# Kernel optimization log

Measured on AMD Instinct MI355X. Metric: run time of the kernel, lower is better.

The kernel has to match this reference:

```python
import jax, jax.numpy as jnp
import numpy as np

N_NODES = 100000
N_REL = 8
IN_DIM = 64
HID = 128
OUT = 64
N_EDGES = 640000


def setup_inputs() -> dict:
    key = jax.random.key(0)
    ks = jax.random.split(key, 24)

    def w(k, shape, fan_in):
        return jax.random.normal(k, shape, jnp.float32) / np.sqrt(fan_in).astype(np.float32)

    inp = {}
    inp["emb"] = jax.random.normal(ks[0], (N_NODES, IN_DIM), jnp.float32)
    dims = [(IN_DIM, HID), (HID, HID), (HID, HID // 2), (HID // 2, OUT)]
    for i, (di, do) in enumerate(dims, 1):
        inp[f"W{i}"] = w(ks[3 * i], (N_REL, di, do), di)      # per-relation weight
        inp[f"R{i}"] = w(ks[3 * i + 1], (di, do), di)          # root weight
        inp[f"B{i}"] = jnp.zeros((do,), jnp.float32)           # bias
    inp["g1"] = jnp.ones((HID,), jnp.float32)
    inp["b1"] = jnp.zeros((HID,), jnp.float32)
    inp["g2"] = jnp.ones((HID,), jnp.float32)
    inp["b2"] = jnp.zeros((HID,), jnp.float32)
    inp["ei"] = jax.random.randint(ks[20], (2, N_EDGES), 0, N_NODES, jnp.int32)
    inp["et"] = jax.random.randint(ks[21], (N_EDGES,), 0, N_REL, jnp.int32)
    return inp


def rgcn(x, ei, et, W, Wr, b):
    # PyG RGCNConv (aggr='mean'): out_i = x_i @ Wroot + b + sum_r mean_{j in N_r(i)} x_j @ W_r
    # Aggregate-then-transform: mean x[src] per (dst, rel) bin, then per-relation GEMM.
    n, r, d = x.shape[0], W.shape[0], x.shape[1]
    src, dst = ei[0], ei[1]
    seg = dst * r + et                                   # combined (node, relation) segment id
    agg = jax.ops.segment_sum(x[src], seg, num_segments=n * r)          # [N*R, d]
    cnt = jax.ops.segment_sum(jnp.ones((src.shape[0],), x.dtype), seg, num_segments=n * r)
    agg = (agg / jnp.maximum(cnt, 1.0)[:, None]).reshape(n, r, d)       # mean per relation
    return jnp.einsum('nri,rio->no', agg, W) + x @ Wr + b


def layer_norm(x, g, b, eps=1e-5):
    mu = jnp.mean(x, axis=-1, keepdims=True)
    var = jnp.mean((x - mu) ** 2, axis=-1, keepdims=True)
    return (x - mu) * jax.lax.rsqrt(var + eps) * g + b


def reference(emb, W1, R1, B1, W2, R2, B2, W3, R3, B3, W4, R4, B4, g1, b1, g2, b2, ei, et):
    # dropout is eval-mode identity
    x = jax.nn.relu(rgcn(emb, ei, et, W1, R1, B1))
    x = layer_norm(x, g1, b1)
    identity = x
    x = jax.nn.relu(rgcn(x, ei, et, W2, R2, B2))
    x = layer_norm(x + identity, g2, b2)
    x = jax.nn.relu(rgcn(x, ei, et, W3, R3, B3))
    return rgcn(x, ei, et, W4, R4, B4)
```

## Files before the change

### kernel.cpp

```cpp
#include <hip/hip_runtime.h>
#include <math.h>

#define NN 100000
#define NR 8
#define NE 640000
#define SEGN (NN * NR)
#define SPB 2048
#define NSB ((SEGN + SPB - 1) / SPB)

#define TILES 1563
#define HT1 782
#define HT2 781
#define HP1 (HT1 * 64)
#define HP2 (HT2 * 64)
#define HPF (TILES * 64)

typedef __attribute__((ext_vector_type(8))) __bf16 bf16x8;
typedef __attribute__((ext_vector_type(4))) float  f32x4;

__device__ __forceinline__ float bf2f(unsigned short b) {
    return __uint_as_float((unsigned)b << 16);
}
__device__ __forceinline__ unsigned short f2bf(float v) {
    __bf16 b = (__bf16)v;
    return __builtin_bit_cast(unsigned short, b);
}


__global__ __launch_bounds__(256) void count_kernel(
    const int* __restrict__ dst, const int* __restrict__ et, unsigned* __restrict__ cnt) {
    int e = blockIdx.x * 256 + threadIdx.x;
    if (e < NE) atomicAdd(&cnt[(size_t)et[e] * NN + dst[e]], 1u);
}

__global__ __launch_bounds__(256) void scan1_kernel(
    const unsigned* __restrict__ cnt, unsigned* __restrict__ bsum) {
    __shared__ unsigned red[256];
    int b = blockIdx.x, t = threadIdx.x;
    int i0 = b * SPB;
    unsigned s = 0;
#pragma unroll
    for (int k = 0; k < SPB / 256; ++k) {
        int i = i0 + k * 256 + t;
        if (i < SEGN) s += cnt[i];
    }
    red[t] = s;
    __syncthreads();
    for (int off = 128; off >= 1; off >>= 1) {
        if (t < off) red[t] += red[t + off];
        __syncthreads();
    }
    if (t == 0) bsum[b] = red[0];
}

__global__ __launch_bounds__(512) void scan2_kernel(
    unsigned* __restrict__ bsum, int* __restrict__ segoff) {
    __shared__ unsigned buf[512];
    int t = threadIdx.x;
    unsigned v = (t < NSB) ? bsum[t] : 0u;
    buf[t] = v;
    __syncthreads();
    for (int off = 1; off < 512; off <<= 1) {
        unsigned w = (t >= off) ? buf[t - off] : 0u;
        __syncthreads();
        buf[t] += w;
        __syncthreads();
    }
    if (t < NSB) bsum[t] = buf[t] - v;
    if (t == 0) segoff[SEGN] = NE;
}

__global__ __launch_bounds__(256) void scan3_kernel(
    const unsigned* __restrict__ cnt, const unsigned* __restrict__ bsum,
    int* __restrict__ segoff) {
    __shared__ unsigned lc[SPB];
    __shared__ unsigned tsum[256];
    int b = blockIdx.x, t = threadIdx.x;
    int i0 = b * SPB;
#pragma unroll
    for (int k = 0; k < SPB / 256; ++k) {
        int i = i0 + k * 256 + t;
        lc[k * 256 + t] = (i < SEGN) ? cnt[i] : 0u;
    }
    __syncthreads();
    unsigned s = 0;
#pragma unroll
    for (int k = 0; k < 8; ++k) s += lc[t * 8 + k];
    tsum[t] = s;
    __syncthreads();
    for (int off = 1; off < 256; off <<= 1) {
        unsigned w = (t >= off) ? tsum[t - off] : 0u;
        __syncthreads();
        tsum[t] += w;
        __syncthreads();
    }
    unsigned base = bsum[b] + tsum[t] - s;
#pragma unroll
    for (int k = 0; k < 8; ++k) {
        unsigned c = lc[t * 8 + k];
        lc[t * 8 + k] = base;
        base += c;
    }
    __syncthreads();
#pragma unroll
    for (int k = 0; k < SPB / 256; ++k) {
        int i = i0 + k * 256 + t;
        if (i < SEGN) segoff[i] = (int)lc[k * 256 + t];
    }
}

__global__ __launch_bounds__(256) void fill_kernel(
    const int* __restrict__ src, const int* __restrict__ dst, const int* __restrict__ et,
    const int* __restrict__ segoff, unsigned* __restrict__ cursor, int* __restrict__ esrc) {
    int e = blockIdx.x * 256 + threadIdx.x;
    if (e >= NE) return;
    int seg = et[e] * NN + dst[e];
    int pos = segoff[seg] + (int)atomicAdd(&cursor[seg], 1u);
    esrc[pos] = src[e];
}


template <int D, int O>
__global__ __launch_bounds__(256) void pack_kernel(
    const float* __restrict__ W, const float* __restrict__ Wr, __bf16* __restrict__ Wp) {
    constexpr int KT = D / 32, NTN = O / 16;
    int idx = blockIdx.x * 256 + threadIdx.x;
    if (idx >= (NR + 1) * KT * NTN * 64) return;
    int l = idx & 63;
    int rest = idx >> 6;
    int nt = rest % NTN; rest /= NTN;
    int kt = rest % KT;
    int r  = rest / KT;
    const float* srcw = (r < NR) ? (W + (size_t)r * D * O) : Wr;
    int n  = nt * 16 + (l & 15);
    int k0 = kt * 32 + (l >> 4) * 8;
    bf16x8 v;
#pragma unroll
    for (int j = 0; j < 8; ++j) v[j] = (__bf16)srcw[(size_t)(k0 + j) * O + n];
    *(bf16x8*)(Wp + (size_t)idx * 8) = v;
}


template <int D, int XF>
__global__ __launch_bounds__(256) void gather_kernel(
    const void* __restrict__ xin, const int* __restrict__ segoff,
    const int* __restrict__ esrc, ushort* __restrict__ agg,
    int base, int HP)
{
    int wv = threadIdx.x >> 6, ln = threadIdx.x & 63;
    int r  = blockIdx.y;
    int i0 = blockIdx.x * 16 + wv * 4;
    int n0 = base + i0;

    const float*   xf = (const float*)xin;
    const ushort*  xb = (const ushort*)xin;
    const ushort2* xs = (const ushort2*)xin;

    if (r < 8) {
        float ax[4] = {0, 0, 0, 0}, ay[4] = {0, 0, 0, 0};
        int eo[5];
#pragma unroll
        for (int k = 0; k <= 4; ++k) {
            int node = n0 + k; if (node > NN) node = NN;
            eo[k] = segoff[r * NN + node];
        }
        for (int ei = eo[0]; ei < eo[4]; ei += 4) {
            int nb = eo[4] - ei; if (nb > 4) nb = 4;
            int ss[4]; float vx[4], vy[4];
#pragma unroll
            for (int b = 0; b < 4; ++b) ss[b] = (b < nb) ? esrc[ei + b] : 0;
#pragma unroll
            for (int b = 0; b < 4; ++b) {
                if (b < nb) {
                    if constexpr (XF == 0) {
                        vx[b] = xf[(size_t)ss[b] * 64 + ln];
                    } else if constexpr (XF == 1) {
                        ushort2 w = xs[(size_t)ss[b] * 64 + ln];
                        vx[b] = bf2f(w.x); vy[b] = bf2f(w.y);
                    } else {
                        vx[b] = bf2f(xb[(size_t)ss[b] * 64 + ln]);
                    }
                }
            }
#pragma unroll
            for (int b = 0; b < 4; ++b) {
                if (b < nb) {
                    int e = ei + b;
                    int k = (e >= eo[1]) + (e >= eo[2]) + (e >= eo[3]);
#pragma unroll
                    for (int kk = 0; kk < 4; ++kk) {
                        ax[kk] += (kk == k) ? vx[b] : 0.0f;
                        if constexpr (D == 128) ay[kk] += (kk == k) ? vy[b] : 0.0f;
                    }
                }
            }
        }
#pragma unroll
        for (int k = 0; k < 4; ++k) {
            int c = eo[k + 1] - eo[k];
            float sc = (c > 0) ? 1.0f / (float)c : 0.0f;
            size_t row = ((size_t)r * HP + i0 + k) * D;
            agg[row + ln] = f2bf(ax[k] * sc);
            if constexpr (D == 128) agg[row + 64 + ln] = f2bf(ay[k] * sc);
        }
    } else {
#pragma unroll
        for (int k = 0; k < 4; ++k) {
            int n = n0 + k;
            float v0 = 0.0f, v1 = 0.0f;
            if (n < NN) {
                if constexpr (XF == 0) {
                    v0 = xf[(size_t)n * 64 + ln];
                } else if constexpr (XF == 1) {
                    ushort2 w = xs[(size_t)n * 64 + ln];
                    v0 = bf2f(w.x); v1 = bf2f(w.y);
                } else {
                    v0 = bf2f(xb[(size_t)n * 64 + ln]);
                }
            }
            size_t row = ((size_t)8 * HP + i0 + k) * D;
            agg[row + ln] = f2bf(v0);
            if constexpr (D == 128) agg[row + 64 + ln] = f2bf(v1);
        }
    }
}


template <int D, int O, int MODE, int OF>
__global__ __launch_bounds__(256) void gemm_layer(
    const ushort* __restrict__ agg, const __bf16* __restrict__ Wp,
    const float* __restrict__ bias, const float* __restrict__ gamma,
    const float* __restrict__ beta, void* __restrict__ outv,
    int base, int HP)
{
    constexpr int KT = D / 32, NTN = O / 16;
    int t = threadIdx.x, wv = t >> 6, ln = t & 63, lg = ln >> 4, lm = ln & 15;
    int i0 = blockIdx.x * 64;

    f32x4 acc[NTN];
#pragma unroll
    for (int nt = 0; nt < NTN; ++nt)
#pragma unroll
        for (int q = 0; q < 4; ++q) acc[nt][q] = 0.0f;

    const ushort* abase = agg + ((size_t)(i0 + wv * 16 + lm)) * D + lg * 8;

#pragma unroll 1
    for (int r = 0; r < 9; ++r) {
        const ushort* ar = abase + (size_t)r * HP * D;
        const __bf16* bp = Wp + (((size_t)(r * KT) * NTN) << 9) + (ln << 3);
#pragma unroll
        for (int kt = 0; kt < KT; ++kt) {
            bf16x8 A = *(const bf16x8*)(ar + kt * 32);
            const __bf16* bpk = bp + (((size_t)(kt * NTN)) << 9);
#pragma unroll
            for (int nt = 0; nt < NTN; ++nt) {
                bf16x8 B = *(const bf16x8*)(bpk + ((size_t)nt << 9));
                acc[nt] = __builtin_amdgcn_mfma_f32_16x16x32_bf16(A, B, acc[nt], 0, 0, 0);
            }
        }
    }

    float bb[NTN], gg[NTN], be[NTN];
#pragma unroll
    for (int nt = 0; nt < NTN; ++nt) {
        bb[nt] = bias[nt * 16 + lm];
        if constexpr (MODE <= 1) {
            gg[nt] = gamma[nt * 16 + lm];
            be[nt] = beta[nt * 16 + lm];
        } else {
            gg[nt] = 0.0f; be[nt] = 0.0f;
        }
    }
    const ushort* rootbase = agg + ((size_t)8 * HP + i0) * D;
#pragma unroll
    for (int q = 0; q < 4; ++q) {
        int row = wv * 16 + lg * 4 + q;
        int n = base + i0 + row;
        float v[NTN];
#pragma unroll
        for (int nt = 0; nt < NTN; ++nt) {
            v[nt] = acc[nt][q] + bb[nt];
            if constexpr (MODE <= 2) v[nt] = fmaxf(v[nt], 0.0f);
            if constexpr (MODE == 1)
                v[nt] += bf2f(rootbase[(size_t)row * D + nt * 16 + lm]);
        }
        if constexpr (MODE <= 1) {
            float s1 = 0.0f, s2 = 0.0f;
#pragma unroll
            for (int nt = 0; nt < NTN; ++nt) { s1 += v[nt]; s2 += v[nt] * v[nt]; }
#pragma unroll
            for (int off = 1; off < 16; off <<= 1) {
                s1 += __shfl_xor(s1, off, 64);
                s2 += __shfl_xor(s2, off, 64);
            }
            float mu  = s1 * (1.0f / O);
            float var = s2 * (1.0f / O) - mu * mu;
            float rs  = rsqrtf(var + 1e-5f);
#pragma unroll
            for (int nt = 0; nt < NTN; ++nt) v[nt] = (v[nt] - mu) * rs * gg[nt] + be[nt];
        }
        if (n < NN) {
            if constexpr (OF == 0) {
#pragma unroll
                for (int nt = 0; nt < NTN; ++nt)
                    ((float*)outv)[(size_t)n * O + nt * 16 + lm] = v[nt];
            } else if constexpr (OF == 1) {
#pragma unroll
                for (int nt = 0; nt < 4; ++nt)
                    ((ushort2*)outv)[(size_t)n * 64 + nt * 16 + lm] =
                        make_ushort2(f2bf(v[nt]), f2bf(v[nt + 4]));
            } else {
#pragma unroll
                for (int nt = 0; nt < NTN; ++nt)
                    ((ushort*)outv)[(size_t)n * 64 + nt * 16 + lm] = f2bf(v[nt]);
            }
        }
    }
}


extern "C" void kernel_launch(void* const* d_in, const int* in_sizes, int n_in,
                              void* d_out, int out_size, void* d_ws, size_t ws_size,
                              hipStream_t stream) {
    const float* emb = (const float*)d_in[0];
    const float* W1  = (const float*)d_in[1];
    const float* R1  = (const float*)d_in[2];
    const float* B1  = (const float*)d_in[3];
    const float* W2  = (const float*)d_in[4];
    const float* R2  = (const float*)d_in[5];
    const float* B2  = (const float*)d_in[6];
    const float* W3  = (const float*)d_in[7];
    const float* R3  = (const float*)d_in[8];
    const float* B3  = (const float*)d_in[9];
    const float* W4  = (const float*)d_in[10];
    const float* R4  = (const float*)d_in[11];
    const float* B4  = (const float*)d_in[12];
    const float* g1  = (const float*)d_in[13];
    const float* b1  = (const float*)d_in[14];
    const float* g2  = (const float*)d_in[15];
    const float* b2  = (const float*)d_in[16];
    const int*   ei  = (const int*)d_in[17];
    const int*   et  = (const int*)d_in[18];
    const int* srcp = ei;
    const int* dstp = ei + NE;

    char* ws = (char*)d_ws;
    if (ws_size < 185734160u) return;
    int*      segoff = (int*)(ws + 0);
    int*      esrc   = (int*)(ws + 3200016);
    __bf16*   Wp1    = (__bf16*)(ws + 5760016);
    __bf16*   Wp2    = (__bf16*)(ws + 5907472);
    __bf16*   Wp3    = (__bf16*)(ws + 6202384);
    __bf16*   Wp4    = (__bf16*)(ws + 6349840);
    void*     x1     = (void*)(ws + 6423568);
    void*     x2     = (void*)(ws + 32023568);
    void*     x3     = (void*)(ws + 57623568);
    ushort*   agg    = (ushort*)(ws + 70423568);
    unsigned* cnt    = (unsigned*)(ws + 70423568);
    unsigned* cursor = (unsigned*)(ws + 73623568);
    unsigned* bsum   = (unsigned*)(ws + 76823568);
    float*    outp   = (float*)d_out;

    hipMemsetAsync(cnt, 0, 3200000, stream);
    hipMemsetAsync(cursor, 0, 3200000, stream);

    count_kernel<<<(NE + 255) / 256, 256, 0, stream>>>(dstp, et, cnt);
    scan1_kernel<<<NSB, 256, 0, stream>>>(cnt, bsum);
    scan2_kernel<<<1, 512, 0, stream>>>(bsum, segoff);
    scan3_kernel<<<NSB, 256, 0, stream>>>(cnt, bsum, segoff);
    fill_kernel<<<(NE + 255) / 256, 256, 0, stream>>>(
        srcp, dstp, et, segoff, cursor, esrc);

    pack_kernel<64, 128><<<(9 * 2 * 8 * 64 + 255) / 256, 256, 0, stream>>>(W1, R1, Wp1);
    pack_kernel<128, 128><<<(9 * 4 * 8 * 64 + 255) / 256, 256, 0, stream>>>(W2, R2, Wp2);
    pack_kernel<128, 64><<<(9 * 4 * 4 * 64 + 255) / 256, 256, 0, stream>>>(W3, R3, Wp3);
    pack_kernel<64, 64><<<(9 * 2 * 4 * 64 + 255) / 256, 256, 0, stream>>>(W4, R4, Wp4);

    gather_kernel<64, 0><<<dim3(HPF / 16, 9), 256, 0, stream>>>(emb, segoff, esrc, agg, 0, HPF);
    gemm_layer<64, 128, 0, 1><<<TILES, 256, 0, stream>>>(agg, Wp1, B1, g1, b1, x1, 0, HPF);

    gather_kernel<128, 1><<<dim3(HP1 / 16, 9), 256, 0, stream>>>(x1, segoff, esrc, agg, 0, HP1);
    gemm_layer<128, 128, 1, 1><<<HT1, 256, 0, stream>>>(agg, Wp2, B2, g2, b2, x2, 0, HP1);
    gather_kernel<128, 1><<<dim3(HP2 / 16, 9), 256, 0, stream>>>(x1, segoff, esrc, agg, HP1, HP2);
    gemm_layer<128, 128, 1, 1><<<HT2, 256, 0, stream>>>(agg, Wp2, B2, g2, b2, x2, HP1, HP2);

    gather_kernel<128, 1><<<dim3(HP1 / 16, 9), 256, 0, stream>>>(x2, segoff, esrc, agg, 0, HP1);
    gemm_layer<128, 64, 2, 2><<<HT1, 256, 0, stream>>>(agg, Wp3, B3, nullptr, nullptr, x3, 0, HP1);
    gather_kernel<128, 1><<<dim3(HP2 / 16, 9), 256, 0, stream>>>(x2, segoff, esrc, agg, HP1, HP2);
    gemm_layer<128, 64, 2, 2><<<HT2, 256, 0, stream>>>(agg, Wp3, B3, nullptr, nullptr, x3, HP1, HP2);

    gather_kernel<64, 2><<<dim3(HPF / 16, 9), 256, 0, stream>>>(x3, segoff, esrc, agg, 0, HPF);
    gemm_layer<64, 64, 3, 0><<<TILES, 256, 0, stream>>>(agg, Wp4, B4, nullptr, nullptr, outp, 0, HPF);
}
```

Before: 824.7 us.

## Interleave bf16 feature layout, pack row index into edge source, use nontemporal memory ops

```diff
diff --git a/kernel.cpp b/kernel.cpp
--- a/kernel.cpp
+++ b/kernel.cpp
@@ -114,9 +114,10 @@
     const int* __restrict__ segoff, unsigned* __restrict__ cursor, int* __restrict__ esrc) {
     int e = blockIdx.x * 256 + threadIdx.x;
     if (e >= NE) return;
-    int seg = et[e] * NN + dst[e];
+    int d = dst[e];
+    int seg = et[e] * NN + d;
     int pos = segoff[seg] + (int)atomicAdd(&cursor[seg], 1u);
-    esrc[pos] = src[e];
+    esrc[pos] = src[e] | ((d & 3) << 17);
 }
 
 
@@ -136,7 +137,11 @@
     int k0 = kt * 32 + (l >> 4) * 8;
     bf16x8 v;
 #pragma unroll
-    for (int j = 0; j < 8; ++j) v[j] = (__bf16)srcw[(size_t)(k0 + j) * O + n];
+    for (int j = 0; j < 8; ++j) {
+        int p  = k0 + j;
+        int kd = (D == 128) ? ((p >> 1) + ((p & 1) << 6)) : p;
+        v[j] = (__bf16)srcw[(size_t)kd * O + n];
+    }
     *(bf16x8*)(Wp + (size_t)idx * 8) = v;
 }
 
@@ -152,9 +157,9 @@
     int i0 = blockIdx.x * 16 + wv * 4;
     int n0 = base + i0;
 
-    const float*   xf = (const float*)xin;
-    const ushort*  xb = (const ushort*)xin;
-    const ushort2* xs = (const ushort2*)xin;
+    const float*    xf = (const float*)xin;
+    const ushort*   xb = (const ushort*)xin;
+    const unsigned* xs = (const unsigned*)xin;
 
     if (r < 8) {
         float ax[4] = {0, 0, 0, 0}, ay[4] = {0, 0, 0, 0};
@@ -166,27 +171,28 @@
         }
         for (int ei = eo[0]; ei < eo[4]; ei += 4) {
             int nb = eo[4] - ei; if (nb > 4) nb = 4;
-            int ss[4]; float vx[4], vy[4];
-#pragma unroll
-            for (int b = 0; b < 4; ++b) ss[b] = (b < nb) ? esrc[ei + b] : 0;
+            int mm[4]; float vx[4], vy[4];
+#pragma unroll
+            for (int b = 0; b < 4; ++b) mm[b] = (b < nb) ? esrc[ei + b] : 0;
 #pragma unroll
             for (int b = 0; b < 4; ++b) {
                 if (b < nb) {
+                    int s = mm[b] & 0x1FFFF;
                     if constexpr (XF == 0) {
-                        vx[b] = xf[(size_t)ss[b] * 64 + ln];
+                        vx[b] = xf[(size_t)s * 64 + ln];
                     } else if constexpr (XF == 1) {
-                        ushort2 w = xs[(size_t)ss[b] * 64 + ln];
-                        vx[b] = bf2f(w.x); vy[b] = bf2f(w.y);
+                        unsigned w = xs[(size_t)s * 64 + ln];
+                        vx[b] = bf2f((unsigned short)(w & 0xFFFFu));
+                        vy[b] = bf2f((unsigned short)(w >> 16));
                     } else {
-                        vx[b] = bf2f(xb[(size_t)ss[b] * 64 + ln]);
+                        vx[b] = bf2f(xb[(size_t)s * 64 + ln]);
                     }
                 }
             }
 #pragma unroll
             for (int b = 0; b < 4; ++b) {
                 if (b < nb) {
-                    int e = ei + b;
-                    int k = (e >= eo[1]) + (e >= eo[2]) + (e >= eo[3]);
+                    int k = mm[b] >> 17;
 #pragma unroll
                     for (int kk = 0; kk < 4; ++kk) {
                         ax[kk] += (kk == k) ? vx[b] : 0.0f;
@@ -200,27 +206,30 @@
             int c = eo[k + 1] - eo[k];
             float sc = (c > 0) ? 1.0f / (float)c : 0.0f;
             size_t row = ((size_t)r * HP + i0 + k) * D;
-            agg[row + ln] = f2bf(ax[k] * sc);
-            if constexpr (D == 128) agg[row + 64 + ln] = f2bf(ay[k] * sc);
+            if constexpr (D == 128) {
+                unsigned st = (unsigned)f2bf(ax[k] * sc) | ((unsigned)f2bf(ay[k] * sc) << 16);
+                __builtin_nontemporal_store(st, (unsigned*)(agg + row) + ln);
+            } else {
+                __builtin_nontemporal_store(f2bf(ax[k] * sc), agg + row + ln);
+            }
         }
     } else {
 #pragma unroll
         for (int k = 0; k < 4; ++k) {
             int n = n0 + k;
-            float v0 = 0.0f, v1 = 0.0f;
-            if (n < NN) {
-                if constexpr (XF == 0) {
-                    v0 = xf[(size_t)n * 64 + ln];
-                } else if constexpr (XF == 1) {
-                    ushort2 w = xs[(size_t)n * 64 + ln];
-                    v0 = bf2f(w.x); v1 = bf2f(w.y);
-                } else {
-                    v0 = bf2f(xb[(size_t)n * 64 + ln]);
+            size_t row = ((size_t)8 * HP + i0 + k) * D;
+            if constexpr (D == 128) {
+                unsigned w = 0;
+                if (n < NN) w = xs[(size_t)n * 64 + ln];
+                __builtin_nontemporal_store(w, (unsigned*)(agg + row) + ln);
+            } else {
+                ushort w = 0;
+                if (n < NN) {
+                    if constexpr (XF == 0) w = f2bf(xf[(size_t)n * 64 + ln]);
+                    else                   w = xb[(size_t)n * 64 + ln];
                 }
-            }
-            size_t row = ((size_t)8 * HP + i0 + k) * D;
-            agg[row + ln] = f2bf(v0);
-            if constexpr (D == 128) agg[row + 64 + ln] = f2bf(v1);
+                __builtin_nontemporal_store(w, agg + row + ln);
+            }
         }
     }
 }
@@ -230,8 +239,8 @@
 __global__ __launch_bounds__(256) void gemm_layer(
     const ushort* __restrict__ agg, const __bf16* __restrict__ Wp,
     const float* __restrict__ bias, const float* __restrict__ gamma,
-    const float* __restrict__ beta, void* __restrict__ outv,
-    int base, int HP)
+    const float* __restrict__ beta, const unsigned* __restrict__ xres,
+    void* __restrict__ outv, int base, int HP)
 {
     constexpr int KT = D / 32, NTN = O / 16;
     int t = threadIdx.x, wv = t >> 6, ln = t & 63, lg = ln >> 4, lm = ln & 15;
@@ -251,7 +260,7 @@
         const __bf16* bp = Wp + (((size_t)(r * KT) * NTN) << 9) + (ln << 3);
 #pragma unroll
         for (int kt = 0; kt < KT; ++kt) {
-            bf16x8 A = *(const bf16x8*)(ar + kt * 32);
+            bf16x8 A = __builtin_nontemporal_load((const bf16x8*)(ar + kt * 32));
             const __bf16* bpk = bp + (((size_t)(kt * NTN)) << 9);
 #pragma unroll
             for (int nt = 0; nt < NTN; ++nt) {
@@ -272,18 +281,20 @@
             gg[nt] = 0.0f; be[nt] = 0.0f;
         }
     }
-    const ushort* rootbase = agg + ((size_t)8 * HP + i0) * D;
 #pragma unroll
     for (int q = 0; q < 4; ++q) {
         int row = wv * 16 + lg * 4 + q;
         int n = base + i0 + row;
+        int nc = (n < NN) ? n : 0;
         float v[NTN];
 #pragma unroll
         for (int nt = 0; nt < NTN; ++nt) {
             v[nt] = acc[nt][q] + bb[nt];
             if constexpr (MODE <= 2) v[nt] = fmaxf(v[nt], 0.0f);
-            if constexpr (MODE == 1)
-                v[nt] += bf2f(rootbase[(size_t)row * D + nt * 16 + lm]);
+            if constexpr (MODE == 1) {
+                unsigned w = xres[(size_t)nc * 64 + (nt & 3) * 16 + lm];
+                v[nt] += bf2f((unsigned short)((nt < 4) ? (w & 0xFFFFu) : (w >> 16)));
+            }
         }
         if constexpr (MODE <= 1) {
             float s1 = 0.0f, s2 = 0.0f;
@@ -304,12 +315,13 @@
             if constexpr (OF == 0) {
 #pragma unroll
                 for (int nt = 0; nt < NTN; ++nt)
-                    ((float*)outv)[(size_t)n * O + nt * 16 + lm] = v[nt];
+                    __builtin_nontemporal_store(
+                        v[nt], (float*)outv + (size_t)n * O + nt * 16 + lm);
             } else if constexpr (OF == 1) {
 #pragma unroll
                 for (int nt = 0; nt < 4; ++nt)
-                    ((ushort2*)outv)[(size_t)n * 64 + nt * 16 + lm] =
-                        make_ushort2(f2bf(v[nt]), f2bf(v[nt + 4]));
+                    ((unsigned*)outv)[(size_t)n * 64 + nt * 16 + lm] =
+                        (unsigned)f2bf(v[nt]) | ((unsigned)f2bf(v[nt + 4]) << 16);
             } else {
 #pragma unroll
                 for (int nt = 0; nt < NTN; ++nt)
@@ -378,18 +390,24 @@
     pack_kernel<64, 64><<<(9 * 2 * 4 * 64 + 255) / 256, 256, 0, stream>>>(W4, R4, Wp4);
 
     gather_kernel<64, 0><<<dim3(HPF / 16, 9), 256, 0, stream>>>(emb, segoff, esrc, agg, 0, HPF);
-    gemm_layer<64, 128, 0, 1><<<TILES, 256, 0, stream>>>(agg, Wp1, B1, g1, b1, x1, 0, HPF);
+    gemm_layer<64, 128, 0, 1><<<TILES, 256, 0, stream>>>(
+        agg, Wp1, B1, g1, b1, nullptr, x1, 0, HPF);
 
     gather_kernel<128, 1><<<dim3(HP1 / 16, 9), 256, 0, stream>>>(x1, segoff, esrc, agg, 0, HP1);
-    gemm_layer<128, 128, 1, 1><<<HT1, 256, 0, stream>>>(agg, Wp2, B2, g2, b2, x2, 0, HP1);
+    gemm_layer<128, 128, 1, 1><<<HT1, 256, 0, stream>>>(
+        agg, Wp2, B2, g2, b2, (const unsigned*)x1, x2, 0, HP1);
     gather_kernel<128, 1><<<dim3(HP2 / 16, 9), 256, 0, stream>>>(x1, segoff, esrc, agg, HP1, HP2);
-    gemm_layer<128, 128, 1, 1><<<HT2, 256, 0, stream>>>(agg, Wp2, B2, g2, b2, x2, HP1, HP2);
+    gemm_layer<128, 128, 1, 1><<<HT2, 256, 0, stream>>>(
+        agg, Wp2, B2, g2, b2, (const unsigned*)x1, x2, HP1, HP2);
 
     gather_kernel<128, 1><<<dim3(HP1 / 16, 9), 256, 0, stream>>>(x2, segoff, esrc, agg, 0, HP1);
-    gemm_layer<128, 64, 2, 2><<<HT1, 256, 0, stream>>>(agg, Wp3, B3, nullptr, nullptr, x3, 0, HP1);
+    gemm_layer<128, 64, 2, 2><<<HT1, 256, 0, stream>>>(
+        agg, Wp3, B3, nullptr, nullptr, nullptr, x3, 0, HP1);
     gather_kernel<128, 1><<<dim3(HP2 / 16, 9), 256, 0, stream>>>(x2, segoff, esrc, agg, HP1, HP2);
-    gemm_layer<128, 64, 2, 2><<<HT2, 256, 0, stream>>>(agg, Wp3, B3, nullptr, nullptr, x3, HP1, HP2);
+    gemm_layer<128, 64, 2, 2><<<HT2, 256, 0, stream>>>(
+        agg, Wp3, B3, nullptr, nullptr, nullptr, x3, HP1, HP2);
 
     gather_kernel<64, 2><<<dim3(HPF / 16, 9), 256, 0, stream>>>(x3, segoff, esrc, agg, 0, HPF);
-    gemm_layer<64, 64, 3, 0><<<TILES, 256, 0, stream>>>(agg, Wp4, B4, nullptr, nullptr, outp, 0, HPF);
-}
+    gemm_layer<64, 64, 3, 0><<<TILES, 256, 0, stream>>>(
+        agg, Wp4, B4, nullptr, nullptr, nullptr, outp, 0, HPF);
+}
```

Result: slower. 864.7 us (+4.9%).
